# Optimization experiments

Hardware: AMD Instinct MI355X
Metric: run time of the kernel (lower is better)

Reference implementation:

```python
import jax, jax.numpy as jnp
import numpy as np

B, N, C, OUT = 4, 512, 128, 128

def setup_inputs() -> dict:
    key = jax.random.key(0)
    k1, k2, k3 = jax.random.split(key, 3)
    adj_matrix = jax.random.bernoulli(k1, 0.1, (B, N, N)).astype(jnp.float32)
    features = jax.random.normal(k2, (B, N, C), dtype=jnp.float32)
    # xavier_uniform for Linear(2C -> OUT): weight stored here as [2C, OUT]
    limit = float(np.sqrt(6.0 / (2 * C + OUT)))
    W = jax.random.uniform(k3, (2 * C, OUT), minval=-limit, maxval=limit, dtype=jnp.float32)
    b = jnp.zeros((OUT,), dtype=jnp.float32)
    return {"adj_matrix": adj_matrix, "features": features, "W": W, "b": b}

def reference(adj_matrix, features, W, b):
    # pooling aggregator: masked max over neighbors (materializes [B,N,N,C], as in source)
    neg_inf = jnp.finfo(features.dtype).min
    mask = (adj_matrix > 0)[..., None]                      # [B,N,N,1]
    feat_nb = jnp.where(mask, features[:, None, :, :], neg_inf)  # [B,N,N,C]
    agg = jnp.max(feat_nb, axis=2)                          # [B,N,C]
    agg = jnp.where(jnp.isfinite(agg), agg, 0.0)
    neigh = jax.nn.relu(agg)
    combined = jnp.concatenate([features, neigh], axis=-1)  # [B,N,2C]
    return jnp.einsum('bnc,co->bno', combined, W) + b       # [B,N,OUT]
```

## Files before the change

kernel.cpp:

```cpp
#include <hip/hip_runtime.h>
#include <hip/hip_bf16.h>
#include <float.h>


#define Bsz 4
#define Nn  512
#define Cc  128
#define OUTn 128
#define NNODES (Bsz * Nn)
#define KK (2 * Cc)
#define ROWP 264

typedef __bf16 bf16x8 __attribute__((ext_vector_type(8)));
typedef float  f32x4  __attribute__((ext_vector_type(4)));

static __device__ __forceinline__ unsigned short f2bf(float x) {
    __hip_bfloat16 h = __float2bfloat16(x);
    return *reinterpret_cast<unsigned short*>(&h);
}
static __device__ __forceinline__ __bf16 f2bf16(float x) {
    unsigned short u = f2bf(x);
    return *reinterpret_cast<__bf16*>(&u);
}

__global__ __launch_bounds__(512) void sage_fused(
    const float* __restrict__ adj,
    const float* __restrict__ feat,
    const float* __restrict__ W,
    const float* __restrict__ bias,
    float* __restrict__ out)
{
    const int w = threadIdx.x >> 6;
    const int l = threadIdx.x & 63;
    const int node = blockIdx.x * 8 + w;
    const int b = node >> 9;
    const int i = node & (Nn - 1);

    __shared__ unsigned short nbr[8][Nn];
    __shared__ unsigned short s_comb[16][ROWP];

    {
        unsigned int* z = (unsigned int*)&s_comb[8][0];
        for (int idx = threadIdx.x; idx < 8 * ROWP / 2; idx += 512) z[idx] = 0u;
    }

    const float* adjrow = adj + (size_t)node * Nn;
    const float2* f2 = (const float2*)(feat + (size_t)b * Nn * Cc);

    int cnt = 0;
    #pragma unroll
    for (int ch = 0; ch < Nn / 64; ++ch) {
        int j = ch * 64 + l;
        float a = adjrow[j];
        unsigned long long mask = __ballot(a > 0.0f);
        int pos = __popcll(mask & ((1ull << l) - 1ull));
        if (a > 0.0f) nbr[w][cnt + pos] = (unsigned short)j;
        cnt += __popcll(mask);
    }

    float m0 = -FLT_MAX, m1 = -FLT_MAX;
    int k = 0;
    for (; k + 4 <= cnt; k += 4) {
        int j0 = nbr[w][k + 0], j1 = nbr[w][k + 1];
        int j2 = nbr[w][k + 2], j3 = nbr[w][k + 3];
        float2 v0 = f2[j0 * 64 + l];
        float2 v1 = f2[j1 * 64 + l];
        float2 v2 = f2[j2 * 64 + l];
        float2 v3 = f2[j3 * 64 + l];
        m0 = fmaxf(m0, fmaxf(fmaxf(v0.x, v1.x), fmaxf(v2.x, v3.x)));
        m1 = fmaxf(m1, fmaxf(fmaxf(v0.y, v1.y), fmaxf(v2.y, v3.y)));
    }
    for (; k < cnt; ++k) {
        int j = nbr[w][k];
        float2 v = f2[j * 64 + l];
        m0 = fmaxf(m0, v.x);
        m1 = fmaxf(m1, v.y);
    }

    float n0 = fmaxf(m0, 0.0f), n1 = fmaxf(m1, 0.0f);
    float2 s = f2[i * 64 + l];

    {
        ushort2* crow = (ushort2*)&s_comb[w][0];
        ushort2 sv; sv.x = f2bf(s.x); sv.y = f2bf(s.y);
        ushort2 nv; nv.x = f2bf(n0);  nv.y = f2bf(n1);
        crow[l]      = sv;
        crow[64 + l] = nv;
    }
    __syncthreads();

    const int nt = w;
    const int frow = l & 15;
    const int koff = (l >> 4) * 8;
    const float* wp = W + nt * 16 + frow;

    f32x4 acc = {0.f, 0.f, 0.f, 0.f};
    #pragma unroll
    for (int ks = 0; ks < KK / 32; ++ks) {
        bf16x8 af = *(const bf16x8*)&s_comb[frow][ks * 32 + koff];
        bf16x8 bfr;
        #pragma unroll
        for (int j = 0; j < 8; ++j) {
            bfr[j] = f2bf16(wp[(size_t)(ks * 32 + koff + j) * OUTn]);
        }
        acc = __builtin_amdgcn_mfma_f32_16x16x32_bf16(af, bfr, acc, 0, 0, 0);
    }

    const int col = l & 15;
    const int r0  = (l >> 4) * 4;
    const float bv = bias[nt * 16 + col];
    #pragma unroll
    for (int r = 0; r < 4; ++r) {
        int row = r0 + r;
        if (row < 8) {
            out[(size_t)(blockIdx.x * 8 + row) * OUTn + nt * 16 + col] = acc[r] + bv;
        }
    }
}

extern "C" void kernel_launch(void* const* d_in, const int* in_sizes, int n_in,
                              void* d_out, int out_size, void* d_ws, size_t ws_size,
                              hipStream_t stream) {
    const float* adj  = (const float*)d_in[0];
    const float* feat = (const float*)d_in[1];
    const float* W    = (const float*)d_in[2];
    const float* bias = (const float*)d_in[3];
    float* out = (float*)d_out;

    sage_fused<<<dim3(NNODES / 8), dim3(512), 0, stream>>>(adj, feat, W, bias, out);
}
```

Baseline: 69.74 us.

## Split neighbor scan across two waves per node and pad gather loop to 8

```diff
diff --git a/kernel.cpp b/kernel.cpp
--- a/kernel.cpp
+++ b/kernel.cpp
@@ -23,65 +23,83 @@
     return *reinterpret_cast<__bf16*>(&u);
 }
 
-__global__ __launch_bounds__(512) void sage_fused(
+__global__ __launch_bounds__(1024) void sage_fused(
     const float* __restrict__ adj,
     const float* __restrict__ feat,
     const float* __restrict__ W,
     const float* __restrict__ bias,
     float* __restrict__ out)
 {
+    const int bid = blockIdx.x;
+    const int mt  = bid >> 1;
+    const int rh  = bid & 1;
     const int w = threadIdx.x >> 6;
     const int l = threadIdx.x & 63;
-    const int node = blockIdx.x * 8 + w;
+
+    __shared__ unsigned short nbr[16][256];
+    __shared__ float2 pm[16][64];
+    __shared__ unsigned short sA[16][ROWP];
+
+    const int slot = w & 7;
+    const int half = w >> 3;
+    const int node = mt * 16 + rh * 8 + slot;
     const int b = node >> 9;
     const int i = node & (Nn - 1);
-
-    __shared__ unsigned short nbr[8][Nn];
-    __shared__ unsigned short s_comb[16][ROWP];
-
-    {
-        unsigned int* z = (unsigned int*)&s_comb[8][0];
-        for (int idx = threadIdx.x; idx < 8 * ROWP / 2; idx += 512) z[idx] = 0u;
-    }
 
     const float* adjrow = adj + (size_t)node * Nn;
     const float2* f2 = (const float2*)(feat + (size_t)b * Nn * Cc);
 
     int cnt = 0;
     #pragma unroll
-    for (int ch = 0; ch < Nn / 64; ++ch) {
-        int j = ch * 64 + l;
+    for (int ch = 0; ch < 4; ++ch) {
+        int j = half * 256 + ch * 64 + l;
         float a = adjrow[j];
         unsigned long long mask = __ballot(a > 0.0f);
         int pos = __popcll(mask & ((1ull << l) - 1ull));
         if (a > 0.0f) nbr[w][cnt + pos] = (unsigned short)j;
         cnt += __popcll(mask);
     }
+    if (cnt > 0) {
+        unsigned short p0 = nbr[w][0];
+        int padded = (cnt + 7) & ~7;
+        if (l < padded - cnt) nbr[w][cnt + l] = p0;
+        cnt = padded;
+    }
 
     float m0 = -FLT_MAX, m1 = -FLT_MAX;
-    int k = 0;
-    for (; k + 4 <= cnt; k += 4) {
+    for (int k = 0; k < cnt; k += 8) {
         int j0 = nbr[w][k + 0], j1 = nbr[w][k + 1];
         int j2 = nbr[w][k + 2], j3 = nbr[w][k + 3];
+        int j4 = nbr[w][k + 4], j5 = nbr[w][k + 5];
+        int j6 = nbr[w][k + 6], j7 = nbr[w][k + 7];
         float2 v0 = f2[j0 * 64 + l];
         float2 v1 = f2[j1 * 64 + l];
         float2 v2 = f2[j2 * 64 + l];
         float2 v3 = f2[j3 * 64 + l];
-        m0 = fmaxf(m0, fmaxf(fmaxf(v0.x, v1.x), fmaxf(v2.x, v3.x)));
-        m1 = fmaxf(m1, fmaxf(fmaxf(v0.y, v1.y), fmaxf(v2.y, v3.y)));
+        float2 v4 = f2[j4 * 64 + l];
+        float2 v5 = f2[j5 * 64 + l];
+        float2 v6 = f2[j6 * 64 + l];
+        float2 v7 = f2[j7 * 64 + l];
+        m0 = fmaxf(m0, fmaxf(fmaxf(fmaxf(v0.x, v1.x), fmaxf(v2.x, v3.x)),
+                             fmaxf(fmaxf(v4.x, v5.x), fmaxf(v6.x, v7.x))));
+        m1 = fmaxf(m1, fmaxf(fmaxf(fmaxf(v0.y, v1.y), fmaxf(v2.y, v3.y)),
+                             fmaxf(fmaxf(v4.y, v5.y), fmaxf(v6.y, v7.y))));
     }
-    for (; k < cnt; ++k) {
-        int j = nbr[w][k];
-        float2 v = f2[j * 64 + l];
-        m0 = fmaxf(m0, v.x);
-        m1 = fmaxf(m1, v.y);
-    }
-
-    float n0 = fmaxf(m0, 0.0f), n1 = fmaxf(m1, 0.0f);
-    float2 s = f2[i * 64 + l];
+    pm[w][l] = make_float2(m0, m1);
 
     {
-        ushort2* crow = (ushort2*)&s_comb[w][0];
+        unsigned int* z = (unsigned int*)&sA[8][0];
+        for (int idx = threadIdx.x; idx < 8 * (ROWP / 2); idx += 1024) z[idx] = 0u;
+    }
+    __syncthreads();
+
+    if (w < 8) {
+        float2 a0 = pm[w][l], a1 = pm[w + 8][l];
+        float n0 = fmaxf(fmaxf(a0.x, a1.x), 0.0f);
+        float n1 = fmaxf(fmaxf(a0.y, a1.y), 0.0f);
+        float2 s = f2[i * 64 + l];
+
+        ushort2* crow = (ushort2*)&sA[w][0];
         ushort2 sv; sv.x = f2bf(s.x); sv.y = f2bf(s.y);
         ushort2 nv; nv.x = f2bf(n0);  nv.y = f2bf(n1);
         crow[l]      = sv;
@@ -89,31 +107,34 @@
     }
     __syncthreads();
 
-    const int nt = w;
-    const int frow = l & 15;
-    const int koff = (l >> 4) * 8;
-    const float* wp = W + nt * 16 + frow;
+    if (w < 8) {
+        const int nt = w;
+        const int frow = l & 15;
+        const int koff = (l >> 4) * 8;
+        const float* wp = W + nt * 16 + frow;
 
-    f32x4 acc = {0.f, 0.f, 0.f, 0.f};
-    #pragma unroll
-    for (int ks = 0; ks < KK / 32; ++ks) {
-        bf16x8 af = *(const bf16x8*)&s_comb[frow][ks * 32 + koff];
-        bf16x8 bfr;
+        f32x4 acc = {0.f, 0.f, 0.f, 0.f};
         #pragma unroll
-        for (int j = 0; j < 8; ++j) {
-            bfr[j] = f2bf16(wp[(size_t)(ks * 32 + koff + j) * OUTn]);
+        for (int ks = 0; ks < KK / 32; ++ks) {
+            bf16x8 af = *(const bf16x8*)&sA[frow][ks * 32 + koff];
+            bf16x8 bfr;
+            #pragma unroll
+            for (int j = 0; j < 8; ++j) {
+                bfr[j] = f2bf16(wp[(size_t)(ks * 32 + koff + j) * OUTn]);
+            }
+            acc = __builtin_amdgcn_mfma_f32_16x16x32_bf16(af, bfr, acc, 0, 0, 0);
         }
-        acc = __builtin_amdgcn_mfma_f32_16x16x32_bf16(af, bfr, acc, 0, 0, 0);
-    }
 
-    const int col = l & 15;
-    const int r0  = (l >> 4) * 4;
-    const float bv = bias[nt * 16 + col];
-    #pragma unroll
-    for (int r = 0; r < 4; ++r) {
-        int row = r0 + r;
-        if (row < 8) {
-            out[(size_t)(blockIdx.x * 8 + row) * OUTn + nt * 16 + col] = acc[r] + bv;
+        const int col = l & 15;
+        const int r0  = (l >> 4) * 4;
+        const float bv = bias[nt * 16 + col];
+        #pragma unroll
+        for (int r = 0; r < 4; ++r) {
+            int row = r0 + r;
+            if (row < 8) {
+                out[(size_t)(mt * 16 + rh * 8 + row) * OUTn + nt * 16 + col]
+                    = acc[r] + bv;
+            }
         }
     }
 }
@@ -127,5 +148,6 @@
     const float* bias = (const float*)d_in[3];
     float* out = (float*)d_out;
 
-    sage_fused<<<dim3(NNODES / 8), dim3(512), 0, stream>>>(adj, feat, W, bias, out);
+    sage_fused<<<dim3(NNODES / 8), dim3(1024), 0, stream>>>(
+        adj, feat, W, bias, out);
 }
```

Measured after the change: 67.12 us. 3.8% less time.
